# Performance work log

Measured on AMD Instinct MI355X. Metric: run time of the kernel, lower is better.

## Reference

```python
import jax, jax.numpy as jnp
import numpy as np
from jax import lax

M_DIM = 128
L1 = L2 = L3 = L4 = 4
L = L1 * L2 * L3 * L4  # 256
RANK = 2
BATCH, D = 4, 16
W = D - RANK + 1  # 15 windows per dim (linear mode, stride 1, drop)


def _make_bbasis():
    # Bbasis[idx, i] = prod_d cos(2*pi*(j_d+1)/(i+2)), idx = ((j1*L2+j2)*L3+j3)*L4+j4
    i = jnp.arange(M_DIM, dtype=jnp.float32)
    def c(Ld):
        j = jnp.arange(D_ := Ld, dtype=jnp.float32)
        return jnp.cos(2.0 * jnp.pi * (j[:, None] + 1.0) / (i[None, :] + 2.0))  # (Ld, m)
    B1, B2, B3, B4 = c(L1), c(L2), c(L3), c(L4)
    Bb = (B1[:, None, None, None, :] * B2[None, :, None, None, :]
          * B3[None, None, :, None, :] * B4[None, None, None, :, :])
    return Bb.reshape(L, M_DIM).astype(jnp.float32)


def setup_inputs() -> dict:
    key = jax.random.key(0)
    k1, k2, k3 = jax.random.split(key, 3)
    vec_arr = jax.random.normal(k1, (BATCH, D, D, D, D, M_DIM), dtype=jnp.float32)
    # M initialized as identity + small noise (nn.init.eye_ is exactly eye; noise keeps grads non-trivial)
    M = jnp.eye(M_DIM, dtype=jnp.float32) + 0.01 * jax.random.normal(k2, (M_DIM, M_DIM), dtype=jnp.float32)
    Acoeff = jax.random.uniform(k3, (M_DIM, L), minval=-0.1, maxval=0.1, dtype=jnp.float32)
    Bbasis = _make_bbasis()
    return {"vec_arr": vec_arr, "M": M, "Acoeff": Acoeff, "Bbasis": Bbasis}


def _basis_index():
    # window coords k_d in [0, W), basis index uses j_d = k_d mod L_d
    k = jnp.arange(W)
    j1 = (k % L1)[:, None, None, None]
    j2 = (k % L2)[None, :, None, None]
    j3 = (k % L3)[None, None, :, None]
    j4 = (k % L4)[None, None, None, :]
    idx = ((j1 * L2 + j2) * L3 + j3) * L4 + j4  # (W,W,W,W)
    return idx.reshape(-1)  # (W^4,)


def reference(vec_arr, M, Acoeff, Bbasis):
    # 4D sliding-window mean (linear mode, stride 1, 'drop'), rank_op='avg'.
    # mean(window @ M.T) == mean(window) @ M.T (linearity), so pool then one GEMM.
    win = (1, RANK, RANK, RANK, RANK, 1)
    pooled = lax.reduce_window(vec_arr, jnp.float32(0.0), lax.add, win,
                               (1, 1, 1, 1, 1, 1), 'VALID') / float(RANK ** 4)
    # agg[b, k1..k4, j] = sum_i pooled[...,i] * M[j,i]  (i.e. x @ M.T)
    agg = jnp.einsum('bwxyzi,ji->bwxyzj', pooled, M)  # (B, W,W,W,W, m)
    agg = agg.reshape(agg.shape[0], -1, M_DIM)        # (B, W^4, m)
    idx = _basis_index()                               # (W^4,)
    # Position-dependent descriptor N(k) = Acoeff[:, idx] * Bbasis[idx, :]
    Nk = Acoeff.T[idx] * Bbasis[idx]                   # (W^4, m)
    return Nk[None, :, :] - agg                        # (B, W^4, m) deviation
```

## Files before the change

### kernel.cpp

```cpp
#include <hip/hip_runtime.h>
#include <hip/hip_bf16.h>
#include <stdint.h>

#define MD     128
#define W4     50625
#define ROWS   202500
#define LBAS   256
#define POOL_THREADS 216000
#define NK_OFF 51840000

typedef __attribute__((ext_vector_type(8))) __bf16 bf16x8;
typedef __attribute__((ext_vector_type(4))) float floatx4;
typedef __attribute__((ext_vector_type(8))) unsigned short ushortx8;

__device__ __forceinline__ float bf2f(unsigned short u){
  union { unsigned int i; float f; } v; v.i = ((unsigned int)u) << 16; return v.f;
}
__device__ __forceinline__ unsigned short f2bf(float x){
  union { float f; unsigned int i; } v; v.f = x;
  unsigned int r = v.i + 0x7FFFu + ((v.i >> 16) & 1u);
  return (unsigned short)(r >> 16);
}
__device__ __forceinline__ int detect_f32(const void* Bbasis){
  return ((const unsigned int*)Bbasis)[0] == 0x3F800000u;
}

__global__ __launch_bounds__(256) void nk_kernel(const void* __restrict__ Acoeff,
                                                 const void* __restrict__ Bbasis,
                                                 float* __restrict__ NkFull){
  int gid = blockIdx.x * 256 + threadIdx.x;
  if (gid >= LBAS * MD) return;
  int idx = gid >> 7;
  int j   = gid & 127;
  float a, b;
  if (detect_f32(Bbasis)){
    a = ((const float*)Acoeff)[j * LBAS + idx];
    b = ((const float*)Bbasis)[idx * MD + j];
  } else {
    a = bf2f(((const unsigned short*)Acoeff)[j * LBAS + idx]);
    b = bf2f(((const unsigned short*)Bbasis)[idx * MD + j]);
  }
  NkFull[gid] = a * b;
}

template<int ISF32>
__device__ __forceinline__ void pool_body(const void* __restrict__ vec,
                                          unsigned short* __restrict__ pooled,
                                          int gid){
  const int ig = gid & 15;
  unsigned int strip = (unsigned int)(gid >> 4);
  const unsigned int w3 = strip % 15u; strip /= 15u;
  const unsigned int w2 = strip % 15u; strip /= 15u;
  const unsigned int w1 = strip % 15u;
  const unsigned int b  = strip / 15u;
  const unsigned int base = b*8388608u + w1*524288u + w2*32768u + w3*2048u
                          + (unsigned int)(ig * 8);
  unsigned int offs[8];
#pragma unroll
  for (int d = 0; d < 8; ++d){
    const unsigned int d1 = (d>>2)&1u, d2 = (d>>1)&1u, d3 = d&1u;
    offs[d] = base + d1*524288u + d2*32768u + d3*2048u;
  }
  const size_t prow0 = (size_t)b*50625u + w1*3375u + w2*225u + w3*15u;
  float prev[8], cur[8];
#pragma unroll 4
  for (int k4 = 0; k4 < 16; ++k4){
#pragma unroll
    for (int e = 0; e < 8; ++e) cur[e] = 0.f;
#pragma unroll
    for (int d = 0; d < 8; ++d){
      const unsigned int off = offs[d] + ((unsigned int)k4 << 7);
      if (ISF32){
        const float* vf = (const float*)vec;
        floatx4 lo = *(const floatx4*)(vf + off);
        floatx4 hi = *(const floatx4*)(vf + off + 4);
#pragma unroll
        for (int e = 0; e < 4; ++e){ cur[e] += lo[e]; cur[4+e] += hi[e]; }
      } else {
        const ushortx8 u = *(const ushortx8*)((const unsigned short*)vec + off);
#pragma unroll
        for (int e = 0; e < 8; ++e) cur[e] += bf2f(u[e]);
      }
    }
    if (k4 > 0){
      ushortx8 ov;
#pragma unroll
      for (int e = 0; e < 8; ++e) ov[e] = f2bf((prev[e] + cur[e]) * 0.0625f);
      *(ushortx8*)(pooled + (prow0 + (unsigned)(k4 - 1)) * 128 + ig * 8) = ov;
    }
#pragma unroll
    for (int e = 0; e < 8; ++e) prev[e] = cur[e];
  }
}

__global__ __launch_bounds__(256) void pool_kernel(const void* __restrict__ vec,
                                                   const void* __restrict__ Bbasis,
                                                   unsigned short* __restrict__ pooled){
  int gid = blockIdx.x * 256 + threadIdx.x;
  if (gid >= POOL_THREADS) return;
  if (detect_f32(Bbasis)) pool_body<1>(vec, pooled, gid);
  else                    pool_body<0>(vec, pooled, gid);
}

__global__ __launch_bounds__(256) void gemm_kernel(const unsigned short* __restrict__ pooled,
                                                   const void* __restrict__ Mmat,
                                                   const float* __restrict__ NkFull,
                                                   const void* __restrict__ Bbasis,
                                                   void* __restrict__ out){
  __shared__ __align__(16) unsigned short sA[128][136];
  __shared__ __align__(16) unsigned short sB[128][136];
  __shared__ int sIdx[128];

  const int tid = threadIdx.x;
  const int p0  = blockIdx.x * 128;
  const int isF32 = detect_f32(Bbasis);

  {
    const int rr  = tid >> 4;
    const int l16 = tid & 15;
#pragma unroll
    for (int r8 = 0; r8 < 8; ++r8){
      const int row = r8 * 16 + rr;
      *(ushortx8*)&sA[row][l16 * 8] =
          *(const ushortx8*)(pooled + (size_t)(p0 + row) * 128 + l16 * 8);
    }
    if (isF32){
      const float* mf = (const float*)Mmat;
#pragma unroll
      for (int r8 = 0; r8 < 8; ++r8){
        const int row = r8 * 16 + rr;
        const float* src = mf + row * 128 + l16 * 8;
        floatx4 lo = *(const floatx4*)src;
        floatx4 hi = *(const floatx4*)(src + 4);
        ushortx8 v;
#pragma unroll
        for (int e = 0; e < 4; ++e){ v[e] = f2bf(lo[e]); v[4+e] = f2bf(hi[e]); }
        *(ushortx8*)&sB[row][l16 * 8] = v;
      }
    } else {
      const unsigned short* mh = (const unsigned short*)Mmat;
#pragma unroll
      for (int r8 = 0; r8 < 8; ++r8){
        const int row = r8 * 16 + rr;
        *(ushortx8*)&sB[row][l16 * 8] = *(const ushortx8*)(mh + row * 128 + l16 * 8);
      }
    }
  }
  if (tid < 128){
    const int p = p0 + tid;
    unsigned int w = (p < ROWS) ? (unsigned int)(p % W4) : 0u;
    const unsigned int w4 = w % 15u; w /= 15u;
    const unsigned int w3 = w % 15u; w /= 15u;
    const unsigned int w2 = w % 15u;
    const unsigned int w1 = w / 15u;
    sIdx[tid] = (int)(((w1 & 3u) << 6) | ((w2 & 3u) << 4) | ((w3 & 3u) << 2) | (w4 & 3u));
  }
  __syncthreads();

  const int wave = tid >> 6;
  const int lane = tid & 63;
  const int quad = lane >> 4;
  const int l16  = lane & 15;

  floatx4 acc[2][8];
#pragma unroll
  for (int rt = 0; rt < 2; ++rt)
#pragma unroll
    for (int c = 0; c < 8; ++c) acc[rt][c] = (floatx4){0.f, 0.f, 0.f, 0.f};

#pragma unroll
  for (int s = 0; s < 4; ++s){
    bf16x8 af[2];
#pragma unroll
    for (int rt = 0; rt < 2; ++rt)
      af[rt] = *(const bf16x8*)&sA[wave * 32 + rt * 16 + l16][s * 32 + quad * 8];
#pragma unroll
    for (int c = 0; c < 8; ++c){
      const bf16x8 bfv = *(const bf16x8*)&sB[c * 16 + l16][s * 32 + quad * 8];
      acc[0][c] = __builtin_amdgcn_mfma_f32_16x16x32_bf16(af[0], bfv, acc[0][c], 0, 0, 0);
      acc[1][c] = __builtin_amdgcn_mfma_f32_16x16x32_bf16(af[1], bfv, acc[1][c], 0, 0, 0);
    }
  }

#pragma unroll
  for (int rt = 0; rt < 2; ++rt){
#pragma unroll
    for (int reg = 0; reg < 4; ++reg){
      const int r = wave * 32 + rt * 16 + quad * 4 + reg;
      const int p = p0 + r;
      if (p < ROWS){
        const float* nkp = NkFull + (sIdx[r] << 7);
        if (isF32){
          float* op = (float*)out + (size_t)p * 128;
#pragma unroll
          for (int c = 0; c < 8; ++c){
            const int j = c * 16 + l16;
            op[j] = nkp[j] - acc[rt][c][reg];
          }
        } else {
          unsigned short* op = (unsigned short*)out + (size_t)p * 128;
#pragma unroll
          for (int c = 0; c < 8; ++c){
            const int j = c * 16 + l16;
            op[j] = f2bf(nkp[j] - acc[rt][c][reg]);
          }
        }
      }
    }
  }
}

extern "C" void kernel_launch(void* const* d_in, const int* in_sizes, int n_in,
                              void* d_out, int out_size, void* d_ws, size_t ws_size,
                              hipStream_t stream) {
  const void* vec = d_in[0];
  const void* Mm  = d_in[1];
  const void* Ac  = d_in[2];
  const void* Bb  = d_in[3];

  unsigned short* pooled = (unsigned short*)d_ws;
  float* NkFull = (float*)((char*)d_ws + NK_OFF);

  nk_kernel<<<128, 256, 0, stream>>>(Ac, Bb, NkFull);
  pool_kernel<<<(POOL_THREADS + 255) / 256, 256, 0, stream>>>(vec, Bb, pooled);
  gemm_kernel<<<(ROWS + 127) / 128, 256, 0, stream>>>(pooled, Mm, NkFull, Bb, d_out);
}
```

Baseline: 291.7 us.

## Slide pool along first dim with 16B loads; stage GEMM epilogue via LDS

The pooling kernel now has each thread slide along the outermost window dimension (k1). Each thread handles 4 channels with one 16-byte fp32 load per corner, and the thread count is doubled to 32 per row. The GEMM epilogue writes accumulators to a shared-memory C tile that is unioned with the A/B tiles, then reads back rows so that Nk loads and output stores are coalesced 16-byte vectors instead of scattered 4-byte stores. The aim is better global memory coalescing on the large output write and more parallelism in pooling, at the cost of an extra LDS round-trip and more pool threads.

After: 283.9 us. 1.03x faster.

```diff
diff --git a/kernel.cpp b/kernel.cpp
--- a/kernel.cpp
+++ b/kernel.cpp
@@ -6,12 +6,13 @@
 #define W4     50625
 #define ROWS   202500
 #define LBAS   256
-#define POOL_THREADS 216000
+#define POOL_THREADS 432000
 #define NK_OFF 51840000
 
 typedef __attribute__((ext_vector_type(8))) __bf16 bf16x8;
 typedef __attribute__((ext_vector_type(4))) float floatx4;
 typedef __attribute__((ext_vector_type(8))) unsigned short ushortx8;
+typedef __attribute__((ext_vector_type(4))) unsigned short ushortx4;
 
 __device__ __forceinline__ float bf2f(unsigned short u){
   union { unsigned int i; float f; } v; v.i = ((unsigned int)u) << 16; return v.f;
@@ -47,49 +48,47 @@
 __device__ __forceinline__ void pool_body(const void* __restrict__ vec,
                                           unsigned short* __restrict__ pooled,
                                           int gid){
-  const int ig = gid & 15;
-  unsigned int strip = (unsigned int)(gid >> 4);
+  const int ig = gid & 31;
+  unsigned int strip = (unsigned int)(gid >> 5);
+  const unsigned int w4 = strip % 15u; strip /= 15u;
   const unsigned int w3 = strip % 15u; strip /= 15u;
-  const unsigned int w2 = strip % 15u; strip /= 15u;
-  const unsigned int w1 = strip % 15u;
+  const unsigned int w2 = strip % 15u;
   const unsigned int b  = strip / 15u;
-  const unsigned int base = b*8388608u + w1*524288u + w2*32768u + w3*2048u
-                          + (unsigned int)(ig * 8);
+  const unsigned int base = b*8388608u + w2*32768u + w3*2048u + w4*128u
+                          + (unsigned int)(ig * 4);
   unsigned int offs[8];
 #pragma unroll
   for (int d = 0; d < 8; ++d){
-    const unsigned int d1 = (d>>2)&1u, d2 = (d>>1)&1u, d3 = d&1u;
-    offs[d] = base + d1*524288u + d2*32768u + d3*2048u;
-  }
-  const size_t prow0 = (size_t)b*50625u + w1*3375u + w2*225u + w3*15u;
-  float prev[8], cur[8];
+    const unsigned int d2 = (d>>2)&1u, d3 = (d>>1)&1u, d4 = d&1u;
+    offs[d] = base + d2*32768u + d3*2048u + d4*128u;
+  }
+  const unsigned int prowB = b*50625u + w2*225u + w3*15u + w4;
+  float prev[4], cur[4];
 #pragma unroll 4
-  for (int k4 = 0; k4 < 16; ++k4){
-#pragma unroll
-    for (int e = 0; e < 8; ++e) cur[e] = 0.f;
+  for (int k1 = 0; k1 < 16; ++k1){
+#pragma unroll
+    for (int e = 0; e < 4; ++e) cur[e] = 0.f;
 #pragma unroll
     for (int d = 0; d < 8; ++d){
-      const unsigned int off = offs[d] + ((unsigned int)k4 << 7);
+      const unsigned int off = offs[d] + (unsigned int)k1 * 524288u;
       if (ISF32){
-        const float* vf = (const float*)vec;
-        floatx4 lo = *(const floatx4*)(vf + off);
-        floatx4 hi = *(const floatx4*)(vf + off + 4);
-#pragma unroll
-        for (int e = 0; e < 4; ++e){ cur[e] += lo[e]; cur[4+e] += hi[e]; }
+        const floatx4 v = *(const floatx4*)((const float*)vec + off);
+#pragma unroll
+        for (int e = 0; e < 4; ++e) cur[e] += v[e];
       } else {
-        const ushortx8 u = *(const ushortx8*)((const unsigned short*)vec + off);
-#pragma unroll
-        for (int e = 0; e < 8; ++e) cur[e] += bf2f(u[e]);
-      }
-    }
-    if (k4 > 0){
-      ushortx8 ov;
-#pragma unroll
-      for (int e = 0; e < 8; ++e) ov[e] = f2bf((prev[e] + cur[e]) * 0.0625f);
-      *(ushortx8*)(pooled + (prow0 + (unsigned)(k4 - 1)) * 128 + ig * 8) = ov;
-    }
-#pragma unroll
-    for (int e = 0; e < 8; ++e) prev[e] = cur[e];
+        const ushortx4 u = *(const ushortx4*)((const unsigned short*)vec + off);
+#pragma unroll
+        for (int e = 0; e < 4; ++e) cur[e] += bf2f(u[e]);
+      }
+    }
+    if (k1 > 0){
+      ushortx4 ov;
+#pragma unroll
+      for (int e = 0; e < 4; ++e) ov[e] = f2bf((prev[e] + cur[e]) * 0.0625f);
+      *(ushortx4*)(pooled + (size_t)(prowB + (unsigned)(k1 - 1) * 3375u) * 128 + ig * 4) = ov;
+    }
+#pragma unroll
+    for (int e = 0; e < 4; ++e) prev[e] = cur[e];
   }
 }
 
@@ -102,13 +101,17 @@
   else                    pool_body<0>(vec, pooled, gid);
 }
 
+union GemmSmem {
+  struct { unsigned short A[128][136]; unsigned short B[128][136]; } ab;
+  float C[128][132];
+};
+
 __global__ __launch_bounds__(256) void gemm_kernel(const unsigned short* __restrict__ pooled,
                                                    const void* __restrict__ Mmat,
                                                    const float* __restrict__ NkFull,
                                                    const void* __restrict__ Bbasis,
                                                    void* __restrict__ out){
-  __shared__ __align__(16) unsigned short sA[128][136];
-  __shared__ __align__(16) unsigned short sB[128][136];
+  __shared__ __align__(16) GemmSmem sm;
   __shared__ int sIdx[128];
 
   const int tid = threadIdx.x;
@@ -121,7 +124,7 @@
 #pragma unroll
     for (int r8 = 0; r8 < 8; ++r8){
       const int row = r8 * 16 + rr;
-      *(ushortx8*)&sA[row][l16 * 8] =
+      *(ushortx8*)&sm.ab.A[row][l16 * 8] =
           *(const ushortx8*)(pooled + (size_t)(p0 + row) * 128 + l16 * 8);
     }
     if (isF32){
@@ -135,14 +138,14 @@
         ushortx8 v;
 #pragma unroll
         for (int e = 0; e < 4; ++e){ v[e] = f2bf(lo[e]); v[4+e] = f2bf(hi[e]); }
-        *(ushortx8*)&sB[row][l16 * 8] = v;
+        *(ushortx8*)&sm.ab.B[row][l16 * 8] = v;
       }
     } else {
       const unsigned short* mh = (const unsigned short*)Mmat;
 #pragma unroll
       for (int r8 = 0; r8 < 8; ++r8){
         const int row = r8 * 16 + rr;
-        *(ushortx8*)&sB[row][l16 * 8] = *(const ushortx8*)(mh + row * 128 + l16 * 8);
+        *(ushortx8*)&sm.ab.B[row][l16 * 8] = *(const ushortx8*)(mh + row * 128 + l16 * 8);
       }
     }
   }
@@ -173,39 +176,48 @@
     bf16x8 af[2];
 #pragma unroll
     for (int rt = 0; rt < 2; ++rt)
-      af[rt] = *(const bf16x8*)&sA[wave * 32 + rt * 16 + l16][s * 32 + quad * 8];
+      af[rt] = *(const bf16x8*)&sm.ab.A[wave * 32 + rt * 16 + l16][s * 32 + quad * 8];
 #pragma unroll
     for (int c = 0; c < 8; ++c){
-      const bf16x8 bfv = *(const bf16x8*)&sB[c * 16 + l16][s * 32 + quad * 8];
+      const bf16x8 bfv = *(const bf16x8*)&sm.ab.B[c * 16 + l16][s * 32 + quad * 8];
       acc[0][c] = __builtin_amdgcn_mfma_f32_16x16x32_bf16(af[0], bfv, acc[0][c], 0, 0, 0);
       acc[1][c] = __builtin_amdgcn_mfma_f32_16x16x32_bf16(af[1], bfv, acc[1][c], 0, 0, 0);
     }
   }
 
+  __syncthreads();
 #pragma unroll
   for (int rt = 0; rt < 2; ++rt){
 #pragma unroll
-    for (int reg = 0; reg < 4; ++reg){
-      const int r = wave * 32 + rt * 16 + quad * 4 + reg;
-      const int p = p0 + r;
-      if (p < ROWS){
-        const float* nkp = NkFull + (sIdx[r] << 7);
-        if (isF32){
-          float* op = (float*)out + (size_t)p * 128;
-#pragma unroll
-          for (int c = 0; c < 8; ++c){
-            const int j = c * 16 + l16;
-            op[j] = nkp[j] - acc[rt][c][reg];
-          }
-        } else {
-          unsigned short* op = (unsigned short*)out + (size_t)p * 128;
-#pragma unroll
-          for (int c = 0; c < 8; ++c){
-            const int j = c * 16 + l16;
-            op[j] = f2bf(nkp[j] - acc[rt][c][reg]);
-          }
-        }
-      }
+    for (int c = 0; c < 8; ++c){
+#pragma unroll
+      for (int reg = 0; reg < 4; ++reg){
+        const int r = wave * 32 + rt * 16 + quad * 4 + reg;
+        sm.C[r][c * 16 + l16] = acc[rt][c][reg];
+      }
+    }
+  }
+  __syncthreads();
+
+  const int rsub = tid >> 5;
+  const int col  = (tid & 31) * 4;
+#pragma unroll
+  for (int k = 0; k < 16; ++k){
+    const int row = k * 8 + rsub;
+    const int p = p0 + row;
+    if (p >= ROWS) continue;
+    const floatx4 v = *(const floatx4*)&sm.C[row][col];
+    const floatx4 nk = *(const floatx4*)(NkFull + (sIdx[row] << 7) + col);
+    floatx4 o;
+#pragma unroll
+    for (int e = 0; e < 4; ++e) o[e] = nk[e] - v[e];
+    if (isF32){
+      *(floatx4*)((float*)out + (size_t)p * 128 + col) = o;
+    } else {
+      ushortx4 ob;
+#pragma unroll
+      for (int e = 0; e < 4; ++e) ob[e] = f2bf(o[e]);
+      *(ushortx4*)((unsigned short*)out + (size_t)p * 128 + col) = ob;
     }
   }
 }
```
